# Kernel tuning notes

Hardware: AMD Instinct MI355X
Metric: run time of the kernel (lower is better)

Reference implementation:

```python
import jax, jax.numpy as jnp
import numpy as np

B, N, A, M, H, KD, VD, O = 256, 2048, 256, 256, 8, 32, 32, 256
EPS = 1e-10

def setup_inputs() -> dict:
    key = jax.random.key(0)
    ks = jax.random.split(key, 8)
    return {
        "q_data": jax.random.normal(ks[0], (B, N, A), dtype=jnp.float32),
        "m_data": jax.random.normal(ks[1], (B, N, M), dtype=jnp.float32),
        "q_mask": jnp.ones((B, N, 1), dtype=jnp.float32),
        "bias": jnp.zeros((B, 1, N), dtype=jnp.float32),
        "query_w": 0.02 * jax.random.normal(ks[2], (A, H, KD), dtype=jnp.float32),
        "key_w": 0.02 * jax.random.normal(ks[3], (M, KD), dtype=jnp.float32),
        "value_w": 0.02 * jax.random.normal(ks[4], (M, VD), dtype=jnp.float32),
        "gating_w": 0.02 * jax.random.normal(ks[5], (A, H, VD), dtype=jnp.float32),
        "gating_b": jnp.zeros((H, VD), dtype=jnp.float32),
        "output_w": 0.02 * jax.random.normal(ks[6], (H, VD, O), dtype=jnp.float32),
        "output_b": jnp.zeros((O,), dtype=jnp.float32),
    }

def reference(q_data, m_data, q_mask, bias, query_w, key_w, value_w,
              gating_w, gating_b, output_w, output_b):
    # masked mean over the query axis: q_mask [B,N,1] broadcasts over channels
    q_avg = jnp.sum(q_mask * q_data, axis=1) / (jnp.sum(q_mask, axis=1) + EPS)  # [B,A]
    kd = query_w.shape[-1]
    q = jnp.einsum('ba,ahc->bhc', q_avg, query_w) * kd ** (-0.5)  # [B,H,KD]
    k = jnp.einsum('bka,ac->bkc', m_data, key_w)                  # [B,N,KD]
    v = jnp.einsum('bka,ac->bkc', m_data, value_w)                # [B,N,VD]
    # the incoming `bias` arg is overwritten by the module, as in the original
    attn_bias = 1e9 * (q_mask[:, None, :, 0] - 1.0)               # [B,1,N]
    logits = jnp.einsum('bhc,bkc->bhk', q, k) + attn_bias         # [B,H,N]
    weights = jax.nn.softmax(logits, axis=-1)
    weighted_avg = jnp.einsum('bhk,bkc->bhc', weights, v)         # [B,H,VD]
    # gating == True
    gate = jax.nn.sigmoid(jnp.einsum('bqc,chv->bqhv', q_data, gating_w) + gating_b)
    gated = weighted_avg[:, None] * gate                          # [B,N,H,VD]
    out = jnp.einsum('bqhc,hco->bqo', gated, output_w) + output_b # [B,N,O]
    return out
```

## Files before the change

### kernel.cpp

```cpp
#include <hip/hip_runtime.h>

#define B_ 256
#define N_ 2048
#define A_ 256
#define M_ 256
#define H_ 8
#define KD_ 32
#define VD_ 32
#define O_ 256

typedef float f32x4 __attribute__((ext_vector_type(4)));
typedef __bf16 bf16x8 __attribute__((ext_vector_type(8)));
typedef unsigned short u16x8 __attribute__((ext_vector_type(8)));

union FragU { u16x8 u; bf16x8 b; };

__device__ __forceinline__ unsigned short f2bf(float f) {
  unsigned int u = __float_as_uint(f);
  u += 0x7fffu + ((u >> 16) & 1u);
  return (unsigned short)(u >> 16);
}
__device__ __forceinline__ float bf2f(unsigned short h) {
  return __uint_as_float(((unsigned int)h) << 16);
}

__global__ void pack_weights(const float* __restrict__ gating_w,
                             const float* __restrict__ output_w,
                             const float* __restrict__ key_w,
                             const float* __restrict__ value_w,
                             unsigned short* __restrict__ wg,
                             unsigned short* __restrict__ wo,
                             unsigned short* __restrict__ wkv) {
  int idx = blockIdx.x * 256 + threadIdx.x;
  int j = idx & 7;
  int lane = (idx >> 3) & 63;
  int rest = idx >> 9;
  int kc = rest & 7, ct = rest >> 3;
  int row = kc * 32 + ((lane >> 4) << 3) + j;
  int col = ct * 16 + (lane & 15);
  wg[idx] = f2bf(gating_w[row * 256 + col]);
  wo[idx] = f2bf(output_w[row * 256 + col]);
  if (idx < 16384) {
    float v = (col < 32) ? key_w[row * 32 + col] : value_w[row * 32 + (col - 32)];
    wkv[idx] = f2bf(v);
  }
}

__global__ void reduce_q(const float* __restrict__ qd, const float* __restrict__ qm,
                         const float* __restrict__ qw, float* __restrict__ q_out) {
  int b = blockIdx.x;
  int t = threadIdx.x;
  int a = t & 255, g = t >> 8;
  const float* qdb = qd + (size_t)b * N_ * A_;
  const float* qmb = qm + (size_t)b * N_;
  float sum = 0.f, msum = 0.f;
  for (int n = g; n < N_; n += 4) {
    float m = qmb[n];
    msum += m;
    sum += m * qdb[(size_t)n * A_ + a];
  }
  __shared__ float s[4][256];
  __shared__ float ms[4];
  __shared__ float qavg[256];
  s[g][a] = sum;
  if (a == 0) ms[g] = msum;
  __syncthreads();
  if (t < 256) {
    float tot = s[0][t] + s[1][t] + s[2][t] + s[3][t];
    float mt = ms[0] + ms[1] + ms[2] + ms[3];
    qavg[t] = tot / (mt + 1e-10f);
  }
  __syncthreads();
  if (t < 256) {
    float acc = 0.f;
    for (int a2 = 0; a2 < 256; a2++) acc += qavg[a2] * qw[a2 * 256 + t];
    q_out[b * 256 + t] = acc * 0.17677669529663687f;
  }
}

__global__ void kv_gemm(const float* __restrict__ md,
                        const unsigned short* __restrict__ wkv,
                        unsigned short* __restrict__ kv) {
  int t = threadIdx.x;
  int w = t >> 6, l = t & 63, q = l >> 4, l15 = l & 15;
  size_t r0 = (size_t)blockIdx.x * 128;
  f32x4 acc[2][4] = {};
  for (int kc = 0; kc < 8; kc++) {
    FragU bfr[4];
#pragma unroll
    for (int ct = 0; ct < 4; ct++)
      bfr[ct].u = *(const u16x8*)(wkv + (((ct * 8 + kc) * 64 + l) << 3));
    FragU af[2];
#pragma unroll
    for (int rt = 0; rt < 2; rt++) {
      size_t row = r0 + (size_t)(w * 32 + rt * 16 + l15);
      const float4* s4 = (const float4*)(md + row * 256 + kc * 32 + q * 8);
      float4 u0 = s4[0], u1 = s4[1];
      af[rt].u = (u16x8){f2bf(u0.x), f2bf(u0.y), f2bf(u0.z), f2bf(u0.w),
                         f2bf(u1.x), f2bf(u1.y), f2bf(u1.z), f2bf(u1.w)};
    }
#pragma unroll
    for (int ct = 0; ct < 4; ct++) {
      acc[0][ct] = __builtin_amdgcn_mfma_f32_16x16x32_bf16(af[0].b, bfr[ct].b, acc[0][ct], 0, 0, 0);
      acc[1][ct] = __builtin_amdgcn_mfma_f32_16x16x32_bf16(af[1].b, bfr[ct].b, acc[1][ct], 0, 0, 0);
    }
  }
#pragma unroll
  for (int rt = 0; rt < 2; rt++)
#pragma unroll
    for (int ct = 0; ct < 4; ct++)
#pragma unroll
      for (int r = 0; r < 4; r++) {
        size_t row = r0 + (size_t)(w * 32 + rt * 16 + q * 4 + r);
        kv[row * 64 + ct * 16 + l15] = f2bf(acc[rt][ct][r]);
      }
}

__global__ void attn_softmax(const unsigned short* __restrict__ kv,
                             const float* __restrict__ qv,
                             const float* __restrict__ qm,
                             float* __restrict__ wa) {
  int b = blockIdx.x, t = threadIdx.x;
  __shared__ float lg[8][2048];
  const float* qb = qv + b * 256;
  const float* qmb = qm + (size_t)b * N_;
  for (int n = t; n < N_; n += 256) {
    const u16x8* kr = (const u16x8*)(kv + ((size_t)(b * N_ + n)) * 64);
    float kf[32];
#pragma unroll
    for (int c8 = 0; c8 < 4; c8++) {
      u16x8 kk = kr[c8];
#pragma unroll
      for (int j = 0; j < 8; j++) kf[c8 * 8 + j] = bf2f(kk[j]);
    }
    float bias_n = 1e9f * (qmb[n] - 1.0f);
#pragma unroll
    for (int h = 0; h < 8; h++) {
      float d = 0.f;
#pragma unroll
      for (int c = 0; c < 32; c++) d += qb[h * 32 + c] * kf[c];
      lg[h][n] = d + bias_n;
    }
  }
  __syncthreads();
  int h = t >> 5, i = t & 31;
  float m = -3.0e38f;
  for (int n = i; n < N_; n += 32) m = fmaxf(m, lg[h][n]);
#pragma unroll
  for (int off = 16; off; off >>= 1) m = fmaxf(m, __shfl_xor(m, off));
  float s = 0.f;
  for (int n = i; n < N_; n += 32) {
    float e = __expf(lg[h][n] - m);
    lg[h][n] = e;
    s += e;
  }
#pragma unroll
  for (int off = 16; off; off >>= 1) s += __shfl_xor(s, off);
  float inv = 1.0f / s;
  __syncthreads();
  float acc = 0.f;
  const unsigned short* vb = kv + ((size_t)b * N_) * 64 + 32 + i;
  for (int n = 0; n < N_; n++) acc += lg[h][n] * bf2f(vb[(size_t)n * 64]);
  wa[b * 256 + t] = acc * inv;
}

__launch_bounds__(256)
__global__ void gate_out(const float* __restrict__ qd,
                         const unsigned short* __restrict__ wg,
                         const unsigned short* __restrict__ wo,
                         const float* __restrict__ wa,
                         const float* __restrict__ gb,
                         const float* __restrict__ ob,
                         float* __restrict__ out) {
  int blk = blockIdx.x;
  int b = blk >> 5, tile = blk & 31;
  int t = threadIdx.x;
  int w = t >> 6, l = t & 63, q = l >> 4, l15 = l & 15;
  __shared__ __attribute__((aligned(16))) unsigned short P[64][264];
  __shared__ __attribute__((aligned(16))) unsigned short Wst[2][8][64][8];
  __shared__ float wa_s[256], gb_s[256], ob_s[256];
  wa_s[t] = wa[b * 256 + t];
  gb_s[t] = gb[t];
  ob_s[t] = ob[t];
  size_t rowbase = (size_t)b * N_ + tile * 64;

  FragU af[8];
  {
    const float* src = qd + (rowbase + (size_t)(w * 16 + l15)) * 256 + q * 8;
#pragma unroll
    for (int kc = 0; kc < 8; kc++) {
      float4 u0 = *(const float4*)(src + kc * 32);
      float4 u1 = *(const float4*)(src + kc * 32 + 4);
      af[kc].u = (u16x8){f2bf(u0.x), f2bf(u0.y), f2bf(u0.z), f2bf(u0.w),
                         f2bf(u1.x), f2bf(u1.y), f2bf(u1.z), f2bf(u1.w)};
    }
  }
  for (int g = 0; g < 8; g++) {
    __syncthreads();
    {
      const u16x8* srcw = (const u16x8*)(wg + g * 8192);
      u16x8* dstw = (u16x8*)&Wst[0][0][0][0];
#pragma unroll
      for (int k = 0; k < 4; k++) dstw[t + k * 256] = srcw[t + k * 256];
    }
    __syncthreads();
    f32x4 acc[2] = {};
#pragma unroll
    for (int kc = 0; kc < 8; kc++) {
      FragU b0, b1;
      b0.u = *(const u16x8*)&Wst[0][kc][l][0];
      b1.u = *(const u16x8*)&Wst[1][kc][l][0];
      acc[0] = __builtin_amdgcn_mfma_f32_16x16x32_bf16(af[kc].b, b0.b, acc[0], 0, 0, 0);
      acc[1] = __builtin_amdgcn_mfma_f32_16x16x32_bf16(af[kc].b, b1.b, acc[1], 0, 0, 0);
    }
#pragma unroll
    for (int ctl = 0; ctl < 2; ctl++) {
      int col = g * 32 + ctl * 16 + l15;
      float wav = wa_s[col], gbv = gb_s[col];
      int prow = w * 16 + q * 4;
#pragma unroll
      for (int r = 0; r < 4; r++) {
        float x = acc[ctl][r] + gbv;
        float gate = 1.0f / (1.0f + __expf(-x));
        P[prow + r][col] = f2bf(wav * gate);
      }
    }
  }
  __syncthreads();
  FragU pf[8];
#pragma unroll
  for (int kc = 0; kc < 8; kc++)
    pf[kc].u = *(const u16x8*)&P[w * 16 + l15][kc * 32 + q * 8];
  for (int g = 0; g < 8; g++) {
    __syncthreads();
    {
      const u16x8* srcw = (const u16x8*)(wo + g * 8192);
      u16x8* dstw = (u16x8*)&Wst[0][0][0][0];
#pragma unroll
      for (int k = 0; k < 4; k++) dstw[t + k * 256] = srcw[t + k * 256];
    }
    __syncthreads();
    f32x4 acc[2] = {};
#pragma unroll
    for (int kc = 0; kc < 8; kc++) {
      FragU b0, b1;
      b0.u = *(const u16x8*)&Wst[0][kc][l][0];
      b1.u = *(const u16x8*)&Wst[1][kc][l][0];
      acc[0] = __builtin_amdgcn_mfma_f32_16x16x32_bf16(pf[kc].b, b0.b, acc[0], 0, 0, 0);
      acc[1] = __builtin_amdgcn_mfma_f32_16x16x32_bf16(pf[kc].b, b1.b, acc[1], 0, 0, 0);
    }
#pragma unroll
    for (int ctl = 0; ctl < 2; ctl++) {
      int col = g * 32 + ctl * 16 + l15;
      float obv = ob_s[col];
      size_t orow = (rowbase + (size_t)(w * 16 + q * 4)) * 256 + col;
#pragma unroll
      for (int r = 0; r < 4; r++)
        out[orow + (size_t)r * 256] = acc[ctl][r] + obv;
    }
  }
}

extern "C" void kernel_launch(void* const* d_in, const int* in_sizes, int n_in,
                              void* d_out, int out_size, void* d_ws, size_t ws_size,
                              hipStream_t stream) {
  const float* q_data   = (const float*)d_in[0];
  const float* m_data   = (const float*)d_in[1];
  const float* q_mask   = (const float*)d_in[2];
  const float* query_w  = (const float*)d_in[4];
  const float* key_w    = (const float*)d_in[5];
  const float* value_w  = (const float*)d_in[6];
  const float* gating_w = (const float*)d_in[7];
  const float* gating_b = (const float*)d_in[8];
  const float* output_w = (const float*)d_in[9];
  const float* output_b = (const float*)d_in[10];
  float* out = (float*)d_out;

  char* ws = (char*)d_ws;
  float* q_ws            = (float*)(ws);
  float* wa_ws           = (float*)(ws + (256 << 10));
  unsigned short* wg_ws  = (unsigned short*)(ws + (512 << 10));
  unsigned short* wo_ws  = (unsigned short*)(ws + (640 << 10));
  unsigned short* wkv_ws = (unsigned short*)(ws + (768 << 10));
  unsigned short* kv_ws  = (unsigned short*)(ws + (800 << 10));

  pack_weights<<<256, 256, 0, stream>>>(gating_w, output_w, key_w, value_w,
                                        wg_ws, wo_ws, wkv_ws);
  reduce_q<<<B_, 1024, 0, stream>>>(q_data, q_mask, query_w, q_ws);
  kv_gemm<<<(B_ * N_) / 128, 256, 0, stream>>>(m_data, wkv_ws, kv_ws);
  attn_softmax<<<B_, 256, 0, stream>>>(kv_ws, q_ws, q_mask, wa_ws);
  gate_out<<<(B_ * N_) / 64, 256, 0, stream>>>(q_data, wg_ws, wo_ws, wa_ws,
                                               gating_b, output_b, out);
}
```

Before: 1.678 ms.

## Fuse gate and output GEMMs per head with double-buffered async weight loads

Result: faster. 1.513 ms (-9.8%).

```diff
diff --git a/kernel.cpp b/kernel.cpp
--- a/kernel.cpp
+++ b/kernel.cpp
@@ -16,12 +16,18 @@
 union FragU { u16x8 u; bf16x8 b; };
 
 __device__ __forceinline__ unsigned short f2bf(float f) {
-  unsigned int u = __float_as_uint(f);
-  u += 0x7fffu + ((u >> 16) & 1u);
-  return (unsigned short)(u >> 16);
+  union { __bf16 b; unsigned short u; } c;
+  c.b = (__bf16)f;
+  return c.u;
 }
 __device__ __forceinline__ float bf2f(unsigned short h) {
   return __uint_as_float(((unsigned int)h) << 16);
+}
+
+__device__ __forceinline__ void gll16(const void* gsrc, void* ldst) {
+  __builtin_amdgcn_global_load_lds(
+      (const __attribute__((address_space(1))) void*)gsrc,
+      (__attribute__((address_space(3))) void*)ldst, 16, 0, 0);
 }
 
 __global__ void pack_weights(const float* __restrict__ gating_w,
@@ -50,24 +56,30 @@
                          const float* __restrict__ qw, float* __restrict__ q_out) {
   int b = blockIdx.x;
   int t = threadIdx.x;
-  int a = t & 255, g = t >> 8;
+  int l = t & 63, g = t >> 6;
   const float* qdb = qd + (size_t)b * N_ * A_;
   const float* qmb = qm + (size_t)b * N_;
-  float sum = 0.f, msum = 0.f;
-  for (int n = g; n < N_; n += 4) {
+  f32x4 sum = {0.f, 0.f, 0.f, 0.f};
+  float msum = 0.f;
+  for (int n = g; n < N_; n += 16) {
     float m = qmb[n];
     msum += m;
-    sum += m * qdb[(size_t)n * A_ + a];
-  }
-  __shared__ float s[4][256];
-  __shared__ float ms[4];
+    f32x4 v = *(const f32x4*)(qdb + (size_t)n * A_ + l * 4);
+    sum += m * v;
+  }
+  __shared__ float s[16][256];
+  __shared__ float ms[16];
   __shared__ float qavg[256];
-  s[g][a] = sum;
-  if (a == 0) ms[g] = msum;
+  *(f32x4*)&s[g][l * 4] = sum;
+  if (l == 0) ms[g] = msum;
   __syncthreads();
   if (t < 256) {
-    float tot = s[0][t] + s[1][t] + s[2][t] + s[3][t];
-    float mt = ms[0] + ms[1] + ms[2] + ms[3];
+    float tot = 0.f;
+#pragma unroll
+    for (int k = 0; k < 16; k++) tot += s[k][t];
+    float mt = 0.f;
+#pragma unroll
+    for (int k = 0; k < 16; k++) mt += ms[k];
     qavg[t] = tot / (mt + 1e-10f);
   }
   __syncthreads();
@@ -122,9 +134,11 @@
                              float* __restrict__ wa) {
   int b = blockIdx.x, t = threadIdx.x;
   __shared__ float lg[8][2048];
+  __shared__ float red[4][256];
+  __shared__ float inv_s[8];
   const float* qb = qv + b * 256;
   const float* qmb = qm + (size_t)b * N_;
-  for (int n = t; n < N_; n += 256) {
+  for (int n = t; n < N_; n += 1024) {
     const u16x8* kr = (const u16x8*)(kv + ((size_t)(b * N_ + n)) * 64);
     float kf[32];
 #pragma unroll
@@ -143,25 +157,37 @@
     }
   }
   __syncthreads();
-  int h = t >> 5, i = t & 31;
-  float m = -3.0e38f;
-  for (int n = i; n < N_; n += 32) m = fmaxf(m, lg[h][n]);
-#pragma unroll
-  for (int off = 16; off; off >>= 1) m = fmaxf(m, __shfl_xor(m, off));
-  float s = 0.f;
-  for (int n = i; n < N_; n += 32) {
-    float e = __expf(lg[h][n] - m);
-    lg[h][n] = e;
-    s += e;
-  }
-#pragma unroll
-  for (int off = 16; off; off >>= 1) s += __shfl_xor(s, off);
-  float inv = 1.0f / s;
-  __syncthreads();
-  float acc = 0.f;
-  const unsigned short* vb = kv + ((size_t)b * N_) * 64 + 32 + i;
-  for (int n = 0; n < N_; n++) acc += lg[h][n] * bf2f(vb[(size_t)n * 64]);
-  wa[b * 256 + t] = acc * inv;
+  if (t < 256) {
+    int h = t >> 5, i = t & 31;
+    float m = -3.0e38f;
+    for (int n = i; n < N_; n += 32) m = fmaxf(m, lg[h][n]);
+#pragma unroll
+    for (int off = 16; off; off >>= 1) m = fmaxf(m, __shfl_xor(m, off));
+    float s = 0.f;
+    for (int n = i; n < N_; n += 32) {
+      float e = __expf(lg[h][n] - m);
+      lg[h][n] = e;
+      s += e;
+    }
+#pragma unroll
+    for (int off = 16; off; off >>= 1) s += __shfl_xor(s, off);
+    if (i == 0) inv_s[h] = 1.0f / s;
+  }
+  __syncthreads();
+  {
+    int c = t & 31, h = (t >> 5) & 7, nq = t >> 8;
+    const unsigned short* vb = kv + ((size_t)b * N_ + nq * 512) * 64 + 32 + c;
+    const float* lgh = &lg[h][nq * 512];
+    float acc = 0.f;
+#pragma unroll 8
+    for (int n = 0; n < 512; n++) acc += lgh[n] * bf2f(vb[(size_t)n * 64]);
+    red[nq][t & 255] = acc;
+  }
+  __syncthreads();
+  if (t < 256) {
+    float r = red[0][t] + red[1][t] + red[2][t] + red[3][t];
+    wa[b * 256 + t] = r * inv_s[t >> 5];
+  }
 }
 
 __launch_bounds__(256)
@@ -176,14 +202,26 @@
   int b = blk >> 5, tile = blk & 31;
   int t = threadIdx.x;
   int w = t >> 6, l = t & 63, q = l >> 4, l15 = l & 15;
-  __shared__ __attribute__((aligned(16))) unsigned short P[64][264];
-  __shared__ __attribute__((aligned(16))) unsigned short Wst[2][8][64][8];
+  __shared__ __attribute__((aligned(16))) unsigned short wst[2][16384];
+  __shared__ __attribute__((aligned(16))) unsigned short Pt[4][16][40];
   __shared__ float wa_s[256], gb_s[256], ob_s[256];
   wa_s[t] = wa[b * 256 + t];
   gb_s[t] = gb[t];
   ob_s[t] = ob[t];
   size_t rowbase = (size_t)b * N_ + tile * 64;
 
+  {
+    const char* wgb = (const char*)wg;
+    const char* wob = (const char*)wo;
+    char* dst = (char*)&wst[0][0];
+#pragma unroll
+    for (int i = 0; i < 4; i++) {
+      int ch = i * 4 + w;
+      gll16(wgb + ch * 1024 + l * 16, dst + ch * 1024);
+      gll16(wob + ch * 8192 + l * 16, dst + 16384 + ch * 1024);
+    }
+  }
+
   FragU af[8];
   {
     const float* src = qd + (rowbase + (size_t)(w * 16 + l15)) * 256 + q * 8;
@@ -195,69 +233,62 @@
                          f2bf(u1.x), f2bf(u1.y), f2bf(u1.z), f2bf(u1.w)};
     }
   }
+  f32x4 acc[16] = {};
+  __syncthreads();
+
   for (int g = 0; g < 8; g++) {
-    __syncthreads();
-    {
-      const u16x8* srcw = (const u16x8*)(wg + g * 8192);
-      u16x8* dstw = (u16x8*)&Wst[0][0][0][0];
-#pragma unroll
-      for (int k = 0; k < 4; k++) dstw[t + k * 256] = srcw[t + k * 256];
-    }
-    __syncthreads();
-    f32x4 acc[2] = {};
+    int cur = g & 1;
+    if (g < 7) {
+      const char* wgb = (const char*)wg + (size_t)(g + 1) * 16384;
+      const char* wob = (const char*)wo + (size_t)(g + 1) * 1024;
+      char* dst = (char*)&wst[cur ^ 1][0];
+#pragma unroll
+      for (int i = 0; i < 4; i++) {
+        int ch = i * 4 + w;
+        gll16(wgb + ch * 1024 + l * 16, dst + ch * 1024);
+        gll16(wob + ch * 8192 + l * 16, dst + 16384 + ch * 1024);
+      }
+    }
+    const unsigned short* wsl = &wst[cur][0];
+    f32x4 gacc[2] = {};
 #pragma unroll
     for (int kc = 0; kc < 8; kc++) {
       FragU b0, b1;
-      b0.u = *(const u16x8*)&Wst[0][kc][l][0];
-      b1.u = *(const u16x8*)&Wst[1][kc][l][0];
-      acc[0] = __builtin_amdgcn_mfma_f32_16x16x32_bf16(af[kc].b, b0.b, acc[0], 0, 0, 0);
-      acc[1] = __builtin_amdgcn_mfma_f32_16x16x32_bf16(af[kc].b, b1.b, acc[1], 0, 0, 0);
+      b0.u = *(const u16x8*)(wsl + ((0 * 8 + kc) * 64 + l) * 8);
+      b1.u = *(const u16x8*)(wsl + ((1 * 8 + kc) * 64 + l) * 8);
+      gacc[0] = __builtin_amdgcn_mfma_f32_16x16x32_bf16(af[kc].b, b0.b, gacc[0], 0, 0, 0);
+      gacc[1] = __builtin_amdgcn_mfma_f32_16x16x32_bf16(af[kc].b, b1.b, gacc[1], 0, 0, 0);
     }
 #pragma unroll
     for (int ctl = 0; ctl < 2; ctl++) {
-      int col = g * 32 + ctl * 16 + l15;
+      int colg = ctl * 16 + l15;
+      int col = g * 32 + colg;
       float wav = wa_s[col], gbv = gb_s[col];
-      int prow = w * 16 + q * 4;
 #pragma unroll
       for (int r = 0; r < 4; r++) {
-        float x = acc[ctl][r] + gbv;
+        float x = gacc[ctl][r] + gbv;
         float gate = 1.0f / (1.0f + __expf(-x));
-        P[prow + r][col] = f2bf(wav * gate);
+        Pt[w][q * 4 + r][colg] = f2bf(wav * gate);
       }
     }
-  }
-  __syncthreads();
-  FragU pf[8];
-#pragma unroll
-  for (int kc = 0; kc < 8; kc++)
-    pf[kc].u = *(const u16x8*)&P[w * 16 + l15][kc * 32 + q * 8];
-  for (int g = 0; g < 8; g++) {
+    FragU pf;
+    pf.u = *(const u16x8*)&Pt[w][l15][q * 8];
+#pragma unroll
+    for (int ct = 0; ct < 16; ct++) {
+      FragU bo;
+      bo.u = *(const u16x8*)(wsl + 8192 + (ct * 64 + l) * 8);
+      acc[ct] = __builtin_amdgcn_mfma_f32_16x16x32_bf16(pf.b, bo.b, acc[ct], 0, 0, 0);
+    }
     __syncthreads();
-    {
-      const u16x8* srcw = (const u16x8*)(wo + g * 8192);
-      u16x8* dstw = (u16x8*)&Wst[0][0][0][0];
-#pragma unroll
-      for (int k = 0; k < 4; k++) dstw[t + k * 256] = srcw[t + k * 256];
-    }
-    __syncthreads();
-    f32x4 acc[2] = {};
-#pragma unroll
-    for (int kc = 0; kc < 8; kc++) {
-      FragU b0, b1;
-      b0.u = *(const u16x8*)&Wst[0][kc][l][0];
-      b1.u = *(const u16x8*)&Wst[1][kc][l][0];
-      acc[0] = __builtin_amdgcn_mfma_f32_16x16x32_bf16(pf[kc].b, b0.b, acc[0], 0, 0, 0);
-      acc[1] = __builtin_amdgcn_mfma_f32_16x16x32_bf16(pf[kc].b, b1.b, acc[1], 0, 0, 0);
-    }
-#pragma unroll
-    for (int ctl = 0; ctl < 2; ctl++) {
-      int col = g * 32 + ctl * 16 + l15;
-      float obv = ob_s[col];
-      size_t orow = (rowbase + (size_t)(w * 16 + q * 4)) * 256 + col;
-#pragma unroll
-      for (int r = 0; r < 4; r++)
-        out[orow + (size_t)r * 256] = acc[ctl][r] + obv;
-    }
+  }
+#pragma unroll
+  for (int ct = 0; ct < 16; ct++) {
+    int col = ct * 16 + l15;
+    float obv = ob_s[col];
+    size_t orow = (rowbase + (size_t)(w * 16 + q * 4)) * 256 + col;
+#pragma unroll
+    for (int r = 0; r < 4; r++)
+      out[orow + (size_t)r * 256] = acc[ct][r] + obv;
   }
 }
 
@@ -288,7 +319,7 @@
                                         wg_ws, wo_ws, wkv_ws);
   reduce_q<<<B_, 1024, 0, stream>>>(q_data, q_mask, query_w, q_ws);
   kv_gemm<<<(B_ * N_) / 128, 256, 0, stream>>>(m_data, wkv_ws, kv_ws);
-  attn_softmax<<<B_, 256, 0, stream>>>(kv_ws, q_ws, q_mask, wa_ws);
+  attn_softmax<<<B_, 1024, 0, stream>>>(kv_ws, q_ws, q_mask, wa_ws);
   gate_out<<<(B_ * N_) / 64, 256, 0, stream>>>(q_data, wg_ws, wo_ws, wa_ws,
                                                gating_b, output_b, out);
 }
```
